# Kernel tuning notes

Measured on AMD Instinct MI355X. Metric: run time of the kernel, lower is better.

Reference implementation:

```python
import jax, jax.numpy as jnp
import numpy as np

N_NODES = 50000
N_EDGES = 600000
D = 128
L = 4
N_GRAPHS = 64
N_PATIENTS = 50
LAMBDA = 1.0

@jax.custom_vjp
def grl(x):
    return x

def _grl_fwd(x):
    return x, None

def _grl_bwd(_, g):
    return (-LAMBDA * g,)

grl.defvjp(_grl_fwd, _grl_bwd)


def setup_inputs() -> dict:
    key = jax.random.key(0)
    ks = jax.random.split(key, 16)
    x = jax.random.normal(ks[0], (N_NODES, D), dtype=jnp.float32)
    edge_index = jax.random.randint(ks[1], (2, N_EDGES), 0, N_NODES, dtype=jnp.int32)
    batch = jnp.sort(jax.random.randint(ks[2], (N_NODES,), 0, N_GRAPHS, dtype=jnp.int32))
    s = 1.0 / np.sqrt(D)
    W_root = jax.random.normal(ks[3], (L, D, D), dtype=jnp.float32) * s
    W_rel = jax.random.normal(ks[4], (L, D, D), dtype=jnp.float32) * s
    b_conv = jnp.zeros((L, D), dtype=jnp.float32)
    ln_gamma = jnp.ones((L, D), dtype=jnp.float32)
    ln_beta = jnp.zeros((L, D), dtype=jnp.float32)
    boundary_W = jax.random.normal(ks[5], (D, 1), dtype=jnp.float32) * s
    boundary_b = jnp.zeros((1,), dtype=jnp.float32)
    dom_W1 = jax.random.normal(ks[6], (D, D // 2), dtype=jnp.float32) * s
    dom_b1 = jnp.zeros((D // 2,), dtype=jnp.float32)
    dom_W2 = jax.random.normal(ks[7], (D // 2, N_PATIENTS), dtype=jnp.float32) * (1.0 / np.sqrt(D // 2))
    dom_b2 = jnp.zeros((N_PATIENTS,), dtype=jnp.float32)
    return {"x": x, "edge_index": edge_index, "batch": batch,
            "W_root": W_root, "W_rel": W_rel, "b_conv": b_conv,
            "ln_gamma": ln_gamma, "ln_beta": ln_beta,
            "boundary_W": boundary_W, "boundary_b": boundary_b,
            "dom_W1": dom_W1, "dom_b1": dom_b1,
            "dom_W2": dom_W2, "dom_b2": dom_b2}


def _layernorm(h, gamma, beta, eps=1e-5):
    mu = jnp.mean(h, axis=-1, keepdims=True)
    var = jnp.var(h, axis=-1, keepdims=True)
    return (h - mu) * jax.lax.rsqrt(var + eps) * gamma + beta


def reference(x, edge_index, batch, W_root, W_rel, b_conv, ln_gamma, ln_beta,
              boundary_W, boundary_b, dom_W1, dom_b1, dom_W2, dom_b2):
    src, dst = edge_index[0], edge_index[1]
    n = x.shape[0]
    for l in range(L):
        x_in = x
        msg = x[src] @ W_rel[l]                                   # [E, D] gather + GEMM
        agg = jax.ops.segment_sum(msg, dst, num_segments=n)        # [N, D] scatter-add
        h = x @ W_root[l] + agg + b_conv[l]
        h = _layernorm(h, ln_gamma[l], ln_beta[l])
        h = jax.nn.elu(h)
        # dropout p=model.dropout in eval mode -> identity
        x = h + x_in                                               # residual (shapes match)
    boundary_logits = (x @ boundary_W + boundary_b)[:, 0]          # [N]
    pooled = jax.ops.segment_sum(x, batch, num_segments=N_GRAPHS)  # [G, D]
    counts = jax.ops.segment_sum(jnp.ones((n, 1), x.dtype), batch, num_segments=N_GRAPHS)
    pooled = pooled / jnp.clip(counts, 1.0)
    r = grl(pooled)                                                # GRL: identity fwd
    h = jax.nn.elu(r @ dom_W1 + dom_b1)                            # Dropout(0.1) eval -> identity
    domain_logits = h @ dom_W2 + dom_b2                            # [G, n_patients]
    return boundary_logits, domain_logits
```

## Files before the change

### kernel.cpp

```cpp
#include <hip/hip_runtime.h>
#include <cstdint>
#include <cstddef>

#define N_NODES   50000
#define N_EDGES   600000
#define DIM       128
#define NLAYERS   4
#define N_GRAPHS  64
#define N_PATIENTS 50

typedef __attribute__((ext_vector_type(8))) __bf16        bf16x8;
typedef __attribute__((ext_vector_type(4))) float         f32x4;
typedef __attribute__((ext_vector_type(4))) unsigned int  u32x4;
typedef __attribute__((ext_vector_type(8))) unsigned short u16x8;

__device__ inline unsigned short f2bf(float f) {
    unsigned u = __builtin_bit_cast(unsigned, f);
    u += 0x7FFFu + ((u >> 16) & 1u);
    return (unsigned short)(u >> 16);
}

__device__ inline float bf2f(unsigned short s) {
    return __builtin_bit_cast(float, (unsigned)s << 16);
}

__device__ inline f32x4 lo4(u16x8 u) {
    f32x4 r;
    r[0] = bf2f(u[0]); r[1] = bf2f(u[1]); r[2] = bf2f(u[2]); r[3] = bf2f(u[3]);
    return r;
}
__device__ inline f32x4 hi4(u16x8 u) {
    f32x4 r;
    r[0] = bf2f(u[4]); r[1] = bf2f(u[5]); r[2] = bf2f(u[6]); r[3] = bf2f(u[7]);
    return r;
}


__global__ void k_count(const int* __restrict__ ei, int* __restrict__ counts) {
    int e = blockIdx.x * 256 + threadIdx.x;
    if (e < N_EDGES) atomicAdd(&counts[ei[N_EDGES + e]], 1);
}

__global__ void k_scan_a(const int* __restrict__ counts, int* __restrict__ incl,
                         int* __restrict__ bsums, int n) {
    __shared__ int s[256];
    int i = blockIdx.x * 256 + threadIdx.x;
    int v = (i < n) ? counts[i] : 0;
    s[threadIdx.x] = v;
    __syncthreads();
    for (int off = 1; off < 256; off <<= 1) {
        int t = (threadIdx.x >= off) ? s[threadIdx.x - off] : 0;
        __syncthreads();
        s[threadIdx.x] += t;
        __syncthreads();
    }
    if (i < n) incl[i] = s[threadIdx.x];
    if (threadIdx.x == 255) bsums[blockIdx.x] = s[255];
}

__global__ void k_scan_b(int* __restrict__ bsums, int nb) {
    __shared__ int s[256];
    int t = threadIdx.x;
    int v = (t < nb) ? bsums[t] : 0;
    s[t] = v;
    __syncthreads();
    for (int off = 1; off < 256; off <<= 1) {
        int u = (t >= off) ? s[t - off] : 0;
        __syncthreads();
        s[t] += u;
        __syncthreads();
    }
    if (t < nb) bsums[t] = s[t];
}

__global__ void k_scan_c(const int* __restrict__ counts, const int* __restrict__ incl,
                         const int* __restrict__ bsums, int* __restrict__ row_ptr,
                         int* __restrict__ cursor, int n) {
    int i = blockIdx.x * 256 + threadIdx.x;
    if (i < n) {
        int off = blockIdx.x ? bsums[blockIdx.x - 1] : 0;
        int ex  = incl[i] - counts[i] + off;
        row_ptr[i] = ex;
        cursor[i]  = ex;
        if (i == n - 1) row_ptr[n] = incl[i] + off;
    }
}

__global__ void k_fill(const int* __restrict__ ei, int* __restrict__ cursor,
                       int* __restrict__ esorted) {
    int e = blockIdx.x * 256 + threadIdx.x;
    if (e < N_EDGES) {
        int d   = ei[N_EDGES + e];
        int pos = atomicAdd(&cursor[d], 1);
        esorted[pos] = ei[e];
    }
}


__global__ void k_prep(const float* __restrict__ x, unsigned short* __restrict__ xb) {
    int idx = blockIdx.x * 256 + threadIdx.x;
    if (idx < N_NODES * DIM / 8) {
        f32x4 v0 = *(const f32x4*)(x + (size_t)idx * 8);
        f32x4 v1 = *(const f32x4*)(x + (size_t)idx * 8 + 4);
        u16x8 o = { f2bf(v0[0]), f2bf(v0[1]), f2bf(v0[2]), f2bf(v0[3]),
                    f2bf(v1[0]), f2bf(v1[1]), f2bf(v1[2]), f2bf(v1[3]) };
        *(u16x8*)(xb + (size_t)idx * 8) = o;
    }
}


__global__ void k_wt(const float* __restrict__ Wroot, const float* __restrict__ Wrel,
                     unsigned short* __restrict__ Wt) {
    int idx = blockIdx.x * 256 + threadIdx.x;
    if (idx < NLAYERS * DIM * 256) {
        int l = idx >> 15;
        int c = (idx >> 8) & 127;
        int k = idx & 255;
        float v = (k < 128) ? Wroot[l * 16384 + k * 128 + c]
                            : Wrel[l * 16384 + (k - 128) * 128 + c];
        Wt[idx] = f2bf(v);
    }
}


__global__ __launch_bounds__(512) void k_layer(
    const float* __restrict__ xin, float* __restrict__ xout,
    const unsigned short* __restrict__ xb,
    unsigned short* __restrict__ xbnext,
    const int* __restrict__ row_ptr, const int* __restrict__ esrc,
    const unsigned short* __restrict__ Wt,
    const float* __restrict__ bconv, const float* __restrict__ gamma,
    const float* __restrict__ beta,
    const float* __restrict__ bW, const float* __restrict__ bb,
    float* __restrict__ boundary, int last)
{
    __shared__ __align__(16) unsigned short x2s[64 * 256];
    __shared__ float rsum[64][2], rsq[64][2], rbl[64][2];
    const int tid     = threadIdx.x;
    const int rowbase = blockIdx.x * 64;

    {
        int r = tid >> 3, q = tid & 7;
        int grow = rowbase + r;
        int rx = (r & 7) << 4;
        if (grow < N_NODES) {
            const unsigned short* xp = xb + (size_t)grow * DIM + q * 16;
            #pragma unroll
            for (int c = 0; c < 2; c++) {
                u16x8 v = *(const u16x8*)(xp + c * 8);
                int byteoff = (r * 512 + q * 32 + c * 16) ^ rx;
                *(u16x8*)((char*)x2s + byteoff) = v;
            }
        } else {
            u16x8 z = { 0, 0, 0, 0, 0, 0, 0, 0 };
            #pragma unroll
            for (int c = 0; c < 2; c++) {
                int byteoff = (r * 512 + q * 32 + c * 16) ^ rx;
                *(u16x8*)((char*)x2s + byteoff) = z;
            }
        }
    }

    {
        int w = tid >> 6, lane = tid & 63;
        int kg = lane >> 4, li = lane & 15;
        #pragma unroll
        for (int rr = 0; rr < 2; ++rr) {
            int i = w * 8 + kg * 2 + rr;
            int grow = rowbase + i;
            f32x4 a0 = 0.f, a1 = 0.f, b0 = 0.f, b1 = 0.f;
            int beg = 0, end = 0;
            if (grow < N_NODES) { beg = row_ptr[grow]; end = row_ptr[grow + 1]; }
            int e = beg;
            for (; e + 3 < end; e += 4) {
                int s0 = esrc[e], s1 = esrc[e + 1], s2 = esrc[e + 2], s3 = esrc[e + 3];
                u16x8 u0 = *(const u16x8*)(xb + (size_t)s0 * DIM + li * 8);
                u16x8 u1 = *(const u16x8*)(xb + (size_t)s1 * DIM + li * 8);
                u16x8 u2 = *(const u16x8*)(xb + (size_t)s2 * DIM + li * 8);
                u16x8 u3 = *(const u16x8*)(xb + (size_t)s3 * DIM + li * 8);
                a0 += lo4(u0); a1 += hi4(u0);
                b0 += lo4(u1); b1 += hi4(u1);
                a0 += lo4(u2); a1 += hi4(u2);
                b0 += lo4(u3); b1 += hi4(u3);
            }
            for (; e < end; ++e) {
                int s0 = esrc[e];
                u16x8 u0 = *(const u16x8*)(xb + (size_t)s0 * DIM + li * 8);
                a0 += lo4(u0); a1 += hi4(u0);
            }
            a0 += b0; a1 += b1;
            u16x8 o = { f2bf(a0[0]), f2bf(a0[1]), f2bf(a0[2]), f2bf(a0[3]),
                        f2bf(a1[0]), f2bf(a1[1]), f2bf(a1[2]), f2bf(a1[3]) };
            int byteoff = (i * 512 + 256 + li * 16) ^ ((i & 7) << 4);
            *(u16x8*)((char*)x2s + byteoff) = o;
        }
    }
    __syncthreads();

    int lane = tid & 63, w = tid >> 6;
    int colb = lane & 15, kg = lane >> 4;
    int rt = w >> 1, ch = w & 1;

    u32x4 araw[8];
    {
        int row  = rt * 16 + colb;
        int base = row * 512 + kg * 16;
        int rx   = (row & 7) << 4;
        #pragma unroll
        for (int ks = 0; ks < 8; ks++) {
            int byteoff = (base + ks * 64) ^ rx;
            araw[ks] = *(const u32x4*)((const char*)x2s + byteoff);
        }
    }

    f32x4 acc[4];
    #pragma unroll
    for (int cb = 0; cb < 4; cb++) acc[cb] = 0.0f;

    #pragma unroll
    for (int cb = 0; cb < 4; cb++) {
        const unsigned short* wp = Wt + ((ch * 64 + cb * 16 + colb) * 256 + kg * 8);
        #pragma unroll
        for (int ks = 0; ks < 8; ks++) {
            u32x4 braw = *(const u32x4*)(wp + ks * 32);
            acc[cb] = __builtin_amdgcn_mfma_f32_16x16x32_bf16(
                __builtin_bit_cast(bf16x8, araw[ks]),
                __builtin_bit_cast(bf16x8, braw), acc[cb], 0, 0, 0);
        }
    }

    float hv[4][4];
    #pragma unroll
    for (int j = 0; j < 4; j++) {
        float ps = 0.f, pq = 0.f;
        #pragma unroll
        for (int cb = 0; cb < 4; cb++) {
            int col = ch * 64 + cb * 16 + colb;
            float h = acc[cb][j] + bconv[col];
            hv[j][cb] = h; ps += h; pq += h * h;
        }
        #pragma unroll
        for (int m = 1; m < 16; m <<= 1) {
            ps += __shfl_xor(ps, m);
            pq += __shfl_xor(pq, m);
        }
        if (colb == 0) {
            int lr = rt * 16 + kg * 4 + j;
            rsum[lr][ch] = ps;
            rsq[lr][ch]  = pq;
        }
    }
    __syncthreads();

    #pragma unroll
    for (int j = 0; j < 4; j++) {
        int lr   = rt * 16 + kg * 4 + j;
        int grow = rowbase + lr;
        float sum = rsum[lr][0] + rsum[lr][1];
        float sq  = rsq[lr][0] + rsq[lr][1];
        float mean = sum * (1.f / 128.f);
        float var  = sq * (1.f / 128.f) - mean * mean;
        float rs   = rsqrtf(var + 1e-5f);
        float bl = 0.f;
        if (grow < N_NODES) {
            #pragma unroll
            for (int cb = 0; cb < 4; cb++) {
                int col  = ch * 64 + cb * 16 + colb;
                float hn = (hv[j][cb] - mean) * rs * gamma[col] + beta[col];
                hn = hn > 0.f ? hn : (expf(hn) - 1.f);
                float xo = hn + xin[(size_t)grow * DIM + col];
                xout[(size_t)grow * DIM + col] = xo;
                if (xbnext) xbnext[(size_t)grow * DIM + col] = f2bf(xo);
                bl += xo * bW[col];
            }
        }
        if (last) {
            #pragma unroll
            for (int m = 1; m < 16; m <<= 1) bl += __shfl_xor(bl, m);
            if (colb == 0) rbl[lr][ch] = bl;
        }
    }
    if (last) {
        __syncthreads();
        if (tid < 64 && rowbase + tid < N_NODES)
            boundary[rowbase + tid] = rbl[tid][0] + rbl[tid][1] + bb[0];
    }
}


__global__ void k_pool(const float* __restrict__ x, const int* __restrict__ batch,
                       float* __restrict__ pooled, int* __restrict__ gcount) {
    __shared__ float s[128];
    int g = blockIdx.x >> 4, q = blockIdx.x & 15;
    int lo = 0, hi = N_NODES;
    while (lo < hi) { int m = (lo + hi) >> 1; if (batch[m] < g) lo = m + 1; else hi = m; }
    int s0 = lo;
    lo = 0; hi = N_NODES;
    while (lo < hi) { int m = (lo + hi) >> 1; if (batch[m] < g + 1) lo = m + 1; else hi = m; }
    int e0  = lo;
    int len = e0 - s0;
    int r0 = s0 + (int)((long long)len * q / 16);
    int r1 = s0 + (int)((long long)len * (q + 1) / 16);
    int col = threadIdx.x & 127, half = threadIdx.x >> 7;
    float acc = 0.f;
    for (int r = r0 + half; r < r1; r += 2) acc += x[(size_t)r * DIM + col];
    if (half) s[col] = acc;
    __syncthreads();
    if (!half) {
        acc += s[col];
        atomicAdd(&pooled[g * DIM + col], acc);
    }
    if (q == 0 && threadIdx.x == 0) gcount[g] = len;
}


__global__ __launch_bounds__(256) void k_dom1(
    const float* __restrict__ pooled, const int* __restrict__ gcount,
    const float* __restrict__ W1, const float* __restrict__ b1,
    float* __restrict__ h1g)
{
    int o = blockIdx.x * 256 + threadIdx.x;
    if (o < 64 * 64) {
        int i = o >> 6, j = o & 63;
        float cnt = (float)gcount[i];
        float rc = 1.f / (cnt < 1.f ? 1.f : cnt);
        float s = b1[j];
        #pragma unroll 8
        for (int k = 0; k < 128; k++) s += pooled[i * 128 + k] * rc * W1[k * 64 + j];
        h1g[o] = s > 0.f ? s : (expf(s) - 1.f);
    }
}

__global__ __launch_bounds__(256) void k_dom2(
    const float* __restrict__ h1g,
    const float* __restrict__ W2, const float* __restrict__ b2,
    float* __restrict__ out)
{
    int o = blockIdx.x * 256 + threadIdx.x;
    if (o < 64 * N_PATIENTS) {
        int i = o / N_PATIENTS, p = o - i * N_PATIENTS;
        float s = b2[p];
        #pragma unroll 8
        for (int k = 0; k < 64; k++) s += h1g[i * 64 + k] * W2[k * N_PATIENTS + p];
        out[o] = s;
    }
}


extern "C" void kernel_launch(void* const* d_in, const int* in_sizes, int n_in,
                              void* d_out, int out_size, void* d_ws, size_t ws_size,
                              hipStream_t stream) {
    const float* x     = (const float*)d_in[0];
    const int*   ei    = (const int*)d_in[1];
    const int*   batch = (const int*)d_in[2];
    const float* Wroot = (const float*)d_in[3];
    const float* Wrel  = (const float*)d_in[4];
    const float* bconv = (const float*)d_in[5];
    const float* gamma = (const float*)d_in[6];
    const float* beta  = (const float*)d_in[7];
    const float* bW    = (const float*)d_in[8];
    const float* bb    = (const float*)d_in[9];
    const float* W1    = (const float*)d_in[10];
    const float* b1    = (const float*)d_in[11];
    const float* W2    = (const float*)d_in[12];
    const float* b2    = (const float*)d_in[13];
    float* out = (float*)d_out;

    char* ws = (char*)d_ws;
    size_t off = 0;
    auto alloc = [&](size_t bytes) -> char* {
        char* p = ws + off;
        off += (bytes + 255) & ~(size_t)255;
        return p;
    };
    float*          xA      = (float*)alloc((size_t)N_NODES * DIM * 4);
    float*          xB      = (float*)alloc((size_t)N_NODES * DIM * 4);
    unsigned short* xbA     = (unsigned short*)alloc((size_t)N_NODES * DIM * 2);
    unsigned short* xbB     = (unsigned short*)alloc((size_t)N_NODES * DIM * 2);
    unsigned short* Wt      = (unsigned short*)alloc((size_t)NLAYERS * DIM * 256 * 2);
    int*            counts  = (int*)alloc((size_t)N_NODES * 4);
    int*            incl    = (int*)alloc((size_t)N_NODES * 4);
    int*            row_ptr = (int*)alloc((size_t)(N_NODES + 1) * 4);
    int*            cursor  = (int*)alloc((size_t)N_NODES * 4);
    int*            esorted = (int*)alloc((size_t)N_EDGES * 4);
    int*            bsums   = (int*)alloc(256 * 4);
    float*          pooled  = (float*)alloc((size_t)N_GRAPHS * DIM * 4);
    int*            gcount  = (int*)alloc((size_t)N_GRAPHS * 4);
    float*          h1g     = (float*)alloc((size_t)64 * 64 * 4);
    (void)ws_size; (void)in_sizes; (void)n_in; (void)out_size;

    hipMemsetAsync(counts, 0, (size_t)N_NODES * 4, stream);
    hipMemsetAsync(pooled, 0, (size_t)N_GRAPHS * DIM * 4, stream);

    k_wt<<<(NLAYERS * DIM * 256 + 255) / 256, 256, 0, stream>>>(Wroot, Wrel, Wt);
    k_prep<<<(N_NODES * DIM / 8 + 255) / 256, 256, 0, stream>>>(x, xbA);
    k_count<<<(N_EDGES + 255) / 256, 256, 0, stream>>>(ei, counts);
    int nb = (N_NODES + 255) / 256;
    k_scan_a<<<nb, 256, 0, stream>>>(counts, incl, bsums, N_NODES);
    k_scan_b<<<1, 256, 0, stream>>>(bsums, nb);
    k_scan_c<<<nb, 256, 0, stream>>>(counts, incl, bsums, row_ptr, cursor, N_NODES);
    k_fill<<<(N_EDGES + 255) / 256, 256, 0, stream>>>(ei, cursor, esorted);

    int lgrid = (N_NODES + 63) / 64;
    const float* xi = x;
    float* xo = xA;
    const unsigned short* xbi = xbA;
    unsigned short* xbo = xbB;
    for (int l = 0; l < NLAYERS; l++) {
        int last = (l == NLAYERS - 1);
        k_layer<<<lgrid, 512, 0, stream>>>(xi, xo, xbi, last ? nullptr : xbo,
                                           row_ptr, esorted, Wt + (size_t)l * DIM * 256,
                                           bconv + l * DIM, gamma + l * DIM, beta + l * DIM,
                                           bW, bb, out, last);
        xi = xo;
        xo = (xo == xA) ? xB : xA;
        const unsigned short* t = xbi; xbi = xbo; xbo = (unsigned short*)t;
    }
    const float* xf = xi;
    k_pool<<<N_GRAPHS * 16, 256, 0, stream>>>(xf, batch, pooled, gcount);
    k_dom1<<<16, 256, 0, stream>>>(pooled, gcount, W1, b1, h1g);
    k_dom2<<<(64 * N_PATIENTS + 255) / 256, 256, 0, stream>>>(h1g, W2, b2, out + N_NODES);
}
```

Measured before the change: 360.1 us.

## Drop fp32 residual stream; keep activations bf16 only and shrink layer tiles

Removes the fp32 copies of the node features. The residual now reads the bf16 input already staged in shared memory, and only a bf16 output is written per layer. Pooling reads the bf16 features two columns at a time. The layer kernel also moves to 32-row tiles with 256 threads and a higher occupancy hint. This cuts global memory traffic per layer, but the residual now accumulates bf16 rounding error across the four layers.

```diff
diff --git a/kernel.cpp b/kernel.cpp
--- a/kernel.cpp
+++ b/kernel.cpp
@@ -8,6 +8,7 @@
 #define NLAYERS   4
 #define N_GRAPHS  64
 #define N_PATIENTS 50
+#define ROWS      32
 
 typedef __attribute__((ext_vector_type(8))) __bf16        bf16x8;
 typedef __attribute__((ext_vector_type(4))) float         f32x4;
@@ -123,8 +124,7 @@
 }
 
 
-__global__ __launch_bounds__(512) void k_layer(
-    const float* __restrict__ xin, float* __restrict__ xout,
+__global__ __launch_bounds__(256, 8) void k_layer(
     const unsigned short* __restrict__ xb,
     unsigned short* __restrict__ xbnext,
     const int* __restrict__ row_ptr, const int* __restrict__ esrc,
@@ -134,10 +134,10 @@
     const float* __restrict__ bW, const float* __restrict__ bb,
     float* __restrict__ boundary, int last)
 {
-    __shared__ __align__(16) unsigned short x2s[64 * 256];
-    __shared__ float rsum[64][2], rsq[64][2], rbl[64][2];
+    __shared__ __align__(16) unsigned short x2s[ROWS * 256];
+    __shared__ float rsum[ROWS][2], rsq[ROWS][2], rbl[ROWS][2];
     const int tid     = threadIdx.x;
-    const int rowbase = blockIdx.x * 64;
+    const int rowbase = blockIdx.x * ROWS;
 
     {
         int r = tid >> 3, q = tid & 7;
@@ -263,14 +263,16 @@
         float rs   = rsqrtf(var + 1e-5f);
         float bl = 0.f;
         if (grow < N_NODES) {
+            int rx = (lr & 7) << 4;
             #pragma unroll
             for (int cb = 0; cb < 4; cb++) {
                 int col  = ch * 64 + cb * 16 + colb;
                 float hn = (hv[j][cb] - mean) * rs * gamma[col] + beta[col];
                 hn = hn > 0.f ? hn : (expf(hn) - 1.f);
-                float xo = hn + xin[(size_t)grow * DIM + col];
-                xout[(size_t)grow * DIM + col] = xo;
-                if (xbnext) xbnext[(size_t)grow * DIM + col] = f2bf(xo);
+                int xoff = (lr * 512 + col * 2) ^ rx;
+                float xi = bf2f(*(const unsigned short*)((const char*)x2s + xoff));
+                float xo = hn + xi;
+                xbnext[(size_t)grow * DIM + col] = f2bf(xo);
                 bl += xo * bW[col];
             }
         }
@@ -282,15 +284,15 @@
     }
     if (last) {
         __syncthreads();
-        if (tid < 64 && rowbase + tid < N_NODES)
+        if (tid < ROWS && rowbase + tid < N_NODES)
             boundary[rowbase + tid] = rbl[tid][0] + rbl[tid][1] + bb[0];
     }
 }
 
 
-__global__ void k_pool(const float* __restrict__ x, const int* __restrict__ batch,
+__global__ void k_pool(const unsigned short* __restrict__ xb, const int* __restrict__ batch,
                        float* __restrict__ pooled, int* __restrict__ gcount) {
-    __shared__ float s[128];
+    __shared__ float2 s[64][4];
     int g = blockIdx.x >> 4, q = blockIdx.x & 15;
     int lo = 0, hi = N_NODES;
     while (lo < hi) { int m = (lo + hi) >> 1; if (batch[m] < g) lo = m + 1; else hi = m; }
@@ -301,14 +303,21 @@
     int len = e0 - s0;
     int r0 = s0 + (int)((long long)len * q / 16);
     int r1 = s0 + (int)((long long)len * (q + 1) / 16);
-    int col = threadIdx.x & 127, half = threadIdx.x >> 7;
-    float acc = 0.f;
-    for (int r = r0 + half; r < r1; r += 2) acc += x[(size_t)r * DIM + col];
-    if (half) s[col] = acc;
+    int cp = threadIdx.x & 63, rp = threadIdx.x >> 6;
+    float ax = 0.f, ay = 0.f;
+    for (int r = r0 + rp; r < r1; r += 4) {
+        unsigned u = *(const unsigned*)(xb + (size_t)r * DIM + cp * 2);
+        ax += bf2f((unsigned short)(u & 0xFFFF));
+        ay += bf2f((unsigned short)(u >> 16));
+    }
+    s[cp][rp] = make_float2(ax, ay);
     __syncthreads();
-    if (!half) {
-        acc += s[col];
-        atomicAdd(&pooled[g * DIM + col], acc);
+    if (rp == 0) {
+        float2 v1 = s[cp][1], v2 = s[cp][2], v3 = s[cp][3];
+        ax += v1.x + v2.x + v3.x;
+        ay += v1.y + v2.y + v3.y;
+        atomicAdd(&pooled[g * DIM + cp * 2], ax);
+        atomicAdd(&pooled[g * DIM + cp * 2 + 1], ay);
     }
     if (q == 0 && threadIdx.x == 0) gcount[g] = len;
 }
@@ -373,8 +382,6 @@
         off += (bytes + 255) & ~(size_t)255;
         return p;
     };
-    float*          xA      = (float*)alloc((size_t)N_NODES * DIM * 4);
-    float*          xB      = (float*)alloc((size_t)N_NODES * DIM * 4);
     unsigned short* xbA     = (unsigned short*)alloc((size_t)N_NODES * DIM * 2);
     unsigned short* xbB     = (unsigned short*)alloc((size_t)N_NODES * DIM * 2);
     unsigned short* Wt      = (unsigned short*)alloc((size_t)NLAYERS * DIM * 256 * 2);
@@ -401,23 +408,18 @@
     k_scan_c<<<nb, 256, 0, stream>>>(counts, incl, bsums, row_ptr, cursor, N_NODES);
     k_fill<<<(N_EDGES + 255) / 256, 256, 0, stream>>>(ei, cursor, esorted);
 
-    int lgrid = (N_NODES + 63) / 64;
-    const float* xi = x;
-    float* xo = xA;
+    int lgrid = (N_NODES + ROWS - 1) / ROWS;
     const unsigned short* xbi = xbA;
     unsigned short* xbo = xbB;
     for (int l = 0; l < NLAYERS; l++) {
         int last = (l == NLAYERS - 1);
-        k_layer<<<lgrid, 512, 0, stream>>>(xi, xo, xbi, last ? nullptr : xbo,
+        k_layer<<<lgrid, 256, 0, stream>>>(xbi, xbo,
                                            row_ptr, esorted, Wt + (size_t)l * DIM * 256,
                                            bconv + l * DIM, gamma + l * DIM, beta + l * DIM,
                                            bW, bb, out, last);
-        xi = xo;
-        xo = (xo == xA) ? xB : xA;
         const unsigned short* t = xbi; xbi = xbo; xbo = (unsigned short*)t;
     }
-    const float* xf = xi;
-    k_pool<<<N_GRAPHS * 16, 256, 0, stream>>>(xf, batch, pooled, gcount);
+    k_pool<<<N_GRAPHS * 16, 256, 0, stream>>>(xbi, batch, pooled, gcount);
     k_dom1<<<16, 256, 0, stream>>>(pooled, gcount, W1, b1, h1g);
     k_dom2<<<(64 * N_PATIENTS + 255) / 256, 256, 0, stream>>>(h1g, W2, b2, out + N_NODES);
 }
```

Measured after the change: 318.3 us. 11.6% less time.
